# Kernel optimization log

Measured on AMD Instinct MI355X. Metric: run time of the kernel, lower is better.

## Reference

```python
import jax, jax.numpy as jnp
import numpy as np
from math import sqrt, log

B, P, C = 8, 256, 512          # batch, patch_size, input_channel
R, M = 64, 256                 # rule_num, model_size
VARPI_1, VARPI_2, TAU_0 = 0.01, 0.001, 0.9
EPS = float(np.finfo(np.float32).tiny)


def setup_inputs() -> dict:
    key = jax.random.key(0)
    ks = jax.random.split(key, 6)

    def xavier(k, shape):
        fan_out, fan_in = shape
        bound = sqrt(6.0 / (fan_in + fan_out))
        return jax.random.uniform(k, shape, jnp.float32, -bound, bound)

    sigma0 = sqrt(-M / (2.0 * (R + 1) * (R + 1) * log(0.5)))
    return {
        "input_data": jax.random.normal(ks[0], (B, P, C), jnp.float32),
        "Wq": xavier(ks[1], (M, P)),      "bq": jnp.zeros((M,), jnp.float32),
        "Wk": xavier(ks[2], (M * R, P)),  "bk": jnp.zeros((M * R,), jnp.float32),
        "Wv": xavier(ks[3], (M * R, P)),  "bv": jnp.zeros((M * R,), jnp.float32),
        "Wo": xavier(ks[4], (P, M)),      "bo": jnp.zeros((P,), jnp.float32),
        "sigma": jnp.full((R, M), sigma0, jnp.float32),
    }


def reference(input_data, Wq, bq, Wk, bk, Wv, bv, Wo, bo, sigma):
    tau = TAU_0 * (1.0 / (R + EPS)) ** (1.0 / M)
    x = jnp.transpose(input_data, (0, 2, 1))            # [B,C,P]
    q = x @ Wq.T + bq                                   # [B,C,M]
    k = (x @ Wk.T + bk).reshape(B, C, R, M)
    v = (x @ Wv.T + bv).reshape(B, C, R, M)

    dist = (q[:, :, None, :] - k) / (sigma + EPS)       # [B,C,R,M]
    fire = jnp.exp(-0.5 / M * jnp.sum(dist * dist, axis=-1)) + EPS   # [B,C,R]
    nfs = fire / (jnp.sum(fire, axis=-1, keepdims=True) + EPS)

    # nucleus-style top-p mask over rule dim (no grad)
    s = jax.lax.stop_gradient(nfs)
    sorted_desc = -jnp.sort(-s, axis=-1)
    err = jnp.cumsum(sorted_desc, axis=-1) - tau
    err = jnp.where(err < 0, jnp.ones_like(err), err)
    idx = jnp.argmin(err, axis=-1)                      # [B,C]
    thresh = jnp.take_along_axis(sorted_desc, idx[..., None], axis=-1)  # [B,C,1]
    mask = (s >= thresh).astype(jnp.float32)

    nfs = nfs * mask
    nfs = nfs / (jnp.sum(nfs, axis=-1, keepdims=True) + EPS)

    pred = jnp.einsum('bcr,bcrm->bcm', nfs, v)          # dropout is identity in eval
    out = jnp.transpose(pred @ Wo.T + bo, (0, 2, 1))    # [B,P,C]

    # constraint loss
    eye = jnp.eye(M, dtype=jnp.float32)
    weight_loss = jnp.linalg.norm(Wq @ Wo - eye)
    bias_loss = jnp.linalg.norm(bq) + jnp.linalg.norm(bo)
    key_l1 = jnp.sum(jnp.abs(Wk)) + jnp.sum(jnp.abs(bk))
    val_l1 = jnp.sum(jnp.abs(Wv)) + jnp.sum(jnp.abs(bv))
    loss = VARPI_1 * (weight_loss + bias_loss) + VARPI_2 * (key_l1 + val_l1)
    return out, loss
```

## Files before the change

### kernel.cpp

```cpp
#include <hip/hip_runtime.h>
#include <math.h>

#define EPS_F 1.1754943508222875e-38f

typedef __attribute__((ext_vector_type(8))) _Float16 half8;
typedef __attribute__((ext_vector_type(4))) float f32x4;
typedef __attribute__((ext_vector_type(8))) unsigned short ushort8;

__device__ __forceinline__ unsigned short f2h(float f) {
  _Float16 h = (_Float16)f;
  return __builtin_bit_cast(unsigned short, h);
}
__device__ __forceinline__ float h2f(unsigned short u) {
  return (float)__builtin_bit_cast(_Float16, u);
}

__device__ __forceinline__ void gload16(const void* g, void* l) {
  __builtin_amdgcn_global_load_lds(
      (const __attribute__((address_space(1))) void*)g,
      (__attribute__((address_space(3))) void*)l, 16, 0, 0);
}

__global__ __launch_bounds__(256) void k_prep_x(const float* __restrict__ in,
                                                unsigned short* __restrict__ x) {
  __shared__ float t[32][33];
  int c0 = blockIdx.x * 32, p0 = blockIdx.y * 32, b = blockIdx.z;
  int tx = threadIdx.x & 31, ty = threadIdx.x >> 5;
#pragma unroll
  for (int i = ty; i < 32; i += 8)
    t[i][tx] = in[(b * 256 + p0 + i) * 512 + c0 + tx];
  __syncthreads();
#pragma unroll
  for (int i = ty; i < 32; i += 8)
    x[(b * 512 + c0 + i) * 256 + p0 + tx] = f2h(t[tx][i]);
}

__global__ __launch_bounds__(256) void k_prepwt(
    const float* __restrict__ Wq, const float* __restrict__ Wk,
    const float* __restrict__ Wv, const float* __restrict__ Wo,
    const float* __restrict__ bq, const float* __restrict__ bk,
    const float* __restrict__ sigma,
    unsigned short* __restrict__ wd, unsigned short* __restrict__ woh,
    unsigned short* __restrict__ wqh, float* __restrict__ bdr,
    float* __restrict__ pbk, unsigned short* __restrict__ wvT,
    unsigned short* __restrict__ woT, float* __restrict__ pbv) {
  __shared__ float t[32][33];
  __shared__ float r1[4];
  const int bid = blockIdx.x;
  const int lane = threadIdx.x & 63, w = threadIdx.x >> 6;
  if (bid < 4096) {
    int gid = bid * 256 + threadIdx.x;
    int i4 = gid * 4;
    int rm = i4 >> 8, p = i4 & 255, m = rm & 255;
    const float4 wk = *(const float4*)(Wk + i4);
    const float4 wq = *(const float4*)(Wq + m * 256 + p);
    float rs = 1.0f / (sigma[rm] + EPS_F);
    ushort4 d;
    d.x = f2h((wq.x - wk.x) * rs); d.y = f2h((wq.y - wk.y) * rs);
    d.z = f2h((wq.z - wk.z) * rs); d.w = f2h((wq.w - wk.w) * rs);
    *(ushort4*)(wd + i4) = d;
    float ak = fabsf(wk.x) + fabsf(wk.y) + fabsf(wk.z) + fabsf(wk.w);
    if (p == 0) bdr[rm] = (bq[m] - bk[rm]) * rs;
    if (gid < 65536) {
      woh[gid] = f2h(Wo[gid]);
      ushort4 q4;
      q4.x = f2h(wq.x); q4.y = f2h(wq.y); q4.z = f2h(wq.z); q4.w = f2h(wq.w);
      *(ushort4*)(wqh + i4) = q4;
    }
#pragma unroll
    for (int dlt = 1; dlt < 64; dlt <<= 1) ak += __shfl_xor(ak, dlt);
    if (lane == 0) r1[w] = ak;
    __syncthreads();
    if (threadIdx.x == 0)
      pbk[bid] = r1[0] + r1[1] + r1[2] + r1[3];
  } else {
    int tt = bid - 4096;
    int z = tt >> 6, rem = tt & 63;
    int bx = rem & 7, by = rem >> 3;
    int tx = threadIdx.x & 31, ty = threadIdx.x >> 5;
    if (z < 64) {
      int p0 = bx * 32, m0 = by * 32, r = z;
      float av = 0.f;
#pragma unroll
      for (int i = ty; i < 32; i += 8) {
        float v = Wv[(size_t)(r * 256 + m0 + i) * 256 + p0 + tx];
        t[i][tx] = v;
        av += fabsf(v);
      }
      __syncthreads();
#pragma unroll
      for (int i = ty; i < 32; i += 8)
        wvT[(size_t)r * 65536 + (p0 + i) * 256 + m0 + tx] = f2h(t[tx][i]);
#pragma unroll
      for (int d = 1; d < 64; d <<= 1) av += __shfl_xor(av, d);
      if (lane == 0) r1[w] = av;
      __syncthreads();
      if (threadIdx.x == 0)
        pbv[r * 64 + by * 8 + bx] = r1[0] + r1[1] + r1[2] + r1[3];
    } else {
      int p0 = bx * 32, m0 = by * 32;
#pragma unroll
      for (int i = ty; i < 32; i += 8)
        t[i][tx] = Wo[(p0 + i) * 256 + m0 + tx];
      __syncthreads();
#pragma unroll
      for (int i = ty; i < 32; i += 8)
        woT[(m0 + i) * 256 + p0 + tx] = f2h(t[tx][i]);
    }
  }
}

__global__ __launch_bounds__(256) void k_gwx(
    const unsigned short* __restrict__ woh, const unsigned short* __restrict__ wvT,
    const unsigned short* __restrict__ wqh, const unsigned short* __restrict__ woT,
    const float* __restrict__ bv,
    unsigned short* __restrict__ G, float* __restrict__ pbw,
    float* __restrict__ hv) {
  __shared__ unsigned short As[128 * 64];
  __shared__ unsigned short Bs[128 * 64];
  __shared__ float red4[4];
  __shared__ float bvl[256];
  const int bid = blockIdx.x;
  const int tid = threadIdx.x, w = tid >> 6, lane = tid & 63;
  const int wr = w >> 1, wc = w & 1, cl = lane & 15, kg = lane >> 4;

  if (bid < 260) {
    const bool isgw = bid < 256;
    const int r = bid >> 2;
    const int rowbase = isgw ? (((bid >> 1) & 1) * 128) : (((bid - 256) >> 1) * 128);
    const int colbase = isgw ? ((bid & 1) * 128) : (((bid - 256) & 1) * 128);
    const unsigned short* Aglob = isgw ? woh : wqh;
    const unsigned short* Bglob = isgw ? (wvT + (size_t)r * 65536) : woT;

    f32x4 acc[4][4];
#pragma unroll
    for (int i = 0; i < 4; ++i)
#pragma unroll
      for (int j = 0; j < 4; ++j) acc[i][j] = (f32x4){0.f, 0.f, 0.f, 0.f};

    for (int tks = 0; tks < 4; ++tks) {
      const int kc = tks * 64;
      __syncthreads();
#pragma unroll
      for (int j = 0; j < 4; ++j) {
        int s = w * 4 + j;
        int ch = s * 64 + lane;
        int row = ch >> 3, c = ch & 7;
        gload16(Aglob + (rowbase + row) * 256 + kc + ((c ^ (row & 7)) << 3),
                As + s * 512);
        gload16(Bglob + (colbase + row) * 256 + kc + ((c ^ (row & 7)) << 3),
                Bs + s * 512);
      }
      __syncthreads();
#pragma unroll
      for (int kk = 0; kk < 2; ++kk) {
        half8 a[4], b[4];
        int g = kk * 4 + kg;
#pragma unroll
        for (int i = 0; i < 4; ++i) {
          int row = wr * 64 + i * 16 + cl;
          a[i] = *(const half8*)(As + row * 64 + ((g ^ (row & 7)) << 3));
        }
#pragma unroll
        for (int j = 0; j < 4; ++j) {
          int n = wc * 64 + j * 16 + cl;
          b[j] = *(const half8*)(Bs + n * 64 + ((g ^ (n & 7)) << 3));
        }
#pragma unroll
        for (int i = 0; i < 4; ++i)
#pragma unroll
          for (int j = 0; j < 4; ++j)
            acc[i][j] = __builtin_amdgcn_mfma_f32_16x16x32_f16(a[i], b[j], acc[i][j], 0, 0, 0);
      }
    }
    if (isgw) {
#pragma unroll
      for (int i = 0; i < 4; ++i)
#pragma unroll
        for (int q = 0; q < 4; ++q) {
          int pr = rowbase + wr * 64 + i * 16 + kg * 4 + q;
#pragma unroll
          for (int j = 0; j < 4; ++j) {
            int pc = colbase + wc * 64 + j * 16 + cl;
            G[(size_t)r * 65536 + pr * 256 + pc] = f2h(acc[i][j][q]);
          }
        }
    } else {
      float s = 0.f;
#pragma unroll
      for (int i = 0; i < 4; ++i)
#pragma unroll
        for (int q = 0; q < 4; ++q) {
          int rg = rowbase + wr * 64 + i * 16 + kg * 4 + q;
#pragma unroll
          for (int j = 0; j < 4; ++j) {
            int cg = colbase + wc * 64 + j * 16 + cl;
            float dd = acc[i][j][q] - (rg == cg ? 1.0f : 0.0f);
            s += dd * dd;
          }
        }
#pragma unroll
      for (int d = 1; d < 64; d <<= 1) s += __shfl_xor(s, d);
      if (lane == 0) red4[w] = s;
      __syncthreads();
      if (tid == 0)
        pbw[bid - 256] = red4[0] + red4[1] + red4[2] + red4[3];
    }
  } else {
    int r = bid - 260;
    bvl[tid] = bv[r * 256 + tid];
    __syncthreads();
    float s = 0.f;
#pragma unroll 8
    for (int c8 = 0; c8 < 32; ++c8) {
      ushort8 wv8 = *(const ushort8*)(woh + tid * 256 + c8 * 8);
#pragma unroll
      for (int e = 0; e < 8; ++e) s = fmaf(h2f(wv8[e]), bvl[c8 * 8 + e], s);
    }
    hv[r * 256 + tid] = s;
  }
}

__global__ __launch_bounds__(256, 2) void k_fire(
    const unsigned short* __restrict__ xh, const unsigned short* __restrict__ wd,
    const float* __restrict__ bdr, float* __restrict__ fire_p) {
  __shared__ unsigned short As[128 * 64];
  __shared__ unsigned short Bs[256 * 64];
  __shared__ float red[128][2];
  const int tid = threadIdx.x, w = tid >> 6, lane = tid & 63;
  const int wr = w >> 1, wc = w & 1, cl = lane & 15, kg = lane >> 4;
  const int wg = blockIdx.x;
  const int swz = (wg & 7) * 256 + (wg >> 3);
  const int bc0 = (swz & 31) * 128, r = swz >> 5;

  float bdrv[8];
#pragma unroll
  for (int j = 0; j < 8; ++j)
    bdrv[j] = bdr[r * 256 + wc * 128 + j * 16 + cl];

  f32x4 acc[4][8];
#pragma unroll
  for (int i = 0; i < 4; ++i)
#pragma unroll
    for (int j = 0; j < 8; ++j) acc[i][j] = (f32x4){0.f, 0.f, 0.f, 0.f};

  for (int t = 0; t < 4; ++t) {
    const int kc = t * 64;
    __syncthreads();
#pragma unroll
    for (int j = 0; j < 4; ++j) {
      int s = w * 4 + j;
      int ch = s * 64 + lane;
      int row = ch >> 3, c = ch & 7;
      gload16(xh + (size_t)(bc0 + row) * 256 + kc + ((c ^ (row & 7)) << 3),
              As + s * 512);
    }
#pragma unroll
    for (int j = 0; j < 8; ++j) {
      int s = w * 8 + j;
      int ch = s * 64 + lane;
      int n = ch >> 3, c = ch & 7;
      gload16(wd + (size_t)r * 65536 + n * 256 + kc + ((c ^ (n & 7)) << 3),
              Bs + s * 512);
    }
    __syncthreads();
#pragma unroll
    for (int kk = 0; kk < 2; ++kk) {
      half8 a[4], b[8];
      int g = kk * 4 + kg;
#pragma unroll
      for (int i = 0; i < 4; ++i) {
        int row = wr * 64 + i * 16 + cl;
        a[i] = *(const half8*)(As + row * 64 + ((g ^ (row & 7)) << 3));
      }
#pragma unroll
      for (int j = 0; j < 8; ++j) {
        int n = wc * 128 + j * 16 + cl;
        b[j] = *(const half8*)(Bs + n * 64 + ((g ^ (n & 7)) << 3));
      }
#pragma unroll
      for (int i = 0; i < 4; ++i)
#pragma unroll
        for (int j = 0; j < 8; ++j)
          acc[i][j] = __builtin_amdgcn_mfma_f32_16x16x32_f16(a[i], b[j], acc[i][j], 0, 0, 0);
    }
  }
  float rowsum[4][4];
#pragma unroll
  for (int i = 0; i < 4; ++i)
#pragma unroll
    for (int q = 0; q < 4; ++q) {
      float s2 = 0.f;
#pragma unroll
      for (int j = 0; j < 8; ++j) {
        float t2 = acc[i][j][q] + bdrv[j];
        s2 += t2 * t2;
      }
      rowsum[i][q] = s2;
    }
#pragma unroll
  for (int dlt = 1; dlt < 16; dlt <<= 1)
#pragma unroll
    for (int i = 0; i < 4; ++i)
#pragma unroll
      for (int q = 0; q < 4; ++q) rowsum[i][q] += __shfl_xor(rowsum[i][q], dlt);
  if (cl == 0) {
#pragma unroll
    for (int i = 0; i < 4; ++i)
#pragma unroll
      for (int q = 0; q < 4; ++q)
        red[wr * 64 + i * 16 + kg * 4 + q][wc] = rowsum[i][q];
  }
  __syncthreads();
  if (tid < 128)
    fire_p[(size_t)(bc0 + tid) * 64 + r] = red[tid][0] + red[tid][1];
}

__global__ __launch_bounds__(256) void k_mask(const float* __restrict__ fire_p,
                                              float* __restrict__ nfs, float tau) {
  int w = threadIdx.x >> 6, lane = threadIdx.x & 63;
  int bc = blockIdx.x * 4 + w;
  size_t ix = (size_t)bc * 64 + lane;
  float f = expf(-0.001953125f * fire_p[ix]) + EPS_F;
  float tot = f;
#pragma unroll
  for (int d = 1; d < 64; d <<= 1) tot += __shfl_xor(tot, d);
  float nf = f / (tot + EPS_F);
  float v = nf;
#pragma unroll
  for (int k = 2; k <= 64; k <<= 1) {
#pragma unroll
    for (int j = 32; j > 0; j >>= 1) {
      if (j >= k) continue;
      float o = __shfl_xor(v, j);
      bool lower = (lane & j) == 0;
      bool desc = (lane & k) == 0;
      float mn = fminf(v, o), mx = fmaxf(v, o);
      v = (desc == lower) ? mx : mn;
    }
  }
  float cs = v;
#pragma unroll
  for (int d = 1; d < 64; d <<= 1) {
    float t = __shfl_up(cs, d);
    if (lane >= d) cs += t;
  }
  float err = cs - tau;
  if (err < 0.f) err = 1.0f;
  float mn = err;
#pragma unroll
  for (int d = 1; d < 64; d <<= 1) mn = fminf(mn, __shfl_xor(mn, d));
  unsigned long long ball = __ballot(err == mn);
  int idx = __ffsll(ball) - 1;
  float thresh = __shfl(v, idx);
  float keep = (nf >= thresh) ? nf : 0.0f;
  float tot2 = keep;
#pragma unroll
  for (int d = 1; d < 64; d <<= 1) tot2 += __shfl_xor(tot2, d);
  nfs[ix] = keep / (tot2 + EPS_F);
}

__global__ __launch_bounds__(512, 4) void k_predg(
    const unsigned short* __restrict__ xh, const unsigned short* __restrict__ G,
    const float* __restrict__ nfs, const float* __restrict__ hv,
    unsigned short* __restrict__ pp) {
  __shared__ unsigned short As[128 * 64];
  __shared__ unsigned short Bs[128 * 64];
  __shared__ float nl[128][9];
  const int tid = threadIdx.x, w = tid >> 6, lane = tid & 63;
  const int wr = w >> 1, wc = w & 1, cl = lane & 15, kg = lane >> 4;
  const int wg = blockIdx.x;
  const int swz = (wg & 7) * 64 + (wg >> 3);
  const int sl = swz >> 6, inner = swz & 63;
  const int bc0 = ((inner >> 1) & 31) * 128, ph = inner & 1;

  for (int e = tid; e < 1024; e += 512)
    nl[e >> 3][e & 7] = nfs[(size_t)(bc0 + (e >> 3)) * 64 + sl * 8 + (e & 7)];

  f32x4 acc[2][4];
#pragma unroll
  for (int i = 0; i < 2; ++i)
#pragma unroll
    for (int j = 0; j < 4; ++j) acc[i][j] = (f32x4){0.f, 0.f, 0.f, 0.f};

  _Float16 nlh[2];
  for (int t = 0; t < 32; ++t) {
    const int rr = t >> 2, kc = (t & 3) * 64;
    __syncthreads();
#pragma unroll
    for (int j = 0; j < 2; ++j) {
      int s = w * 2 + j;
      int ch = s * 64 + lane;
      int row = ch >> 3, c = ch & 7;
      gload16(xh + (size_t)(bc0 + row) * 256 + kc + ((c ^ (row & 7)) << 3),
              As + s * 512);
      gload16(G + (size_t)(sl * 8 + rr) * 65536 + (ph * 128 + row) * 256 + kc +
                  ((c ^ (row & 7)) << 3),
              Bs + s * 512);
    }
    __syncthreads();
    if ((t & 3) == 0) {
#pragma unroll
      for (int i = 0; i < 2; ++i)
        nlh[i] = (_Float16)nl[wr * 32 + i * 16 + cl][rr];
    }
#pragma unroll
    for (int kk = 0; kk < 2; ++kk) {
      half8 a[2], b[4];
      int g = kk * 4 + kg;
#pragma unroll
      for (int i = 0; i < 2; ++i) {
        int row = wr * 32 + i * 16 + cl;
        a[i] = *(const half8*)(As + row * 64 + ((g ^ (row & 7)) << 3));
        a[i] = a[i] * nlh[i];
      }
#pragma unroll
      for (int j = 0; j < 4; ++j) {
        int n = wc * 64 + j * 16 + cl;
        b[j] = *(const half8*)(Bs + n * 64 + ((g ^ (n & 7)) << 3));
      }
#pragma unroll
      for (int i = 0; i < 2; ++i)
#pragma unroll
        for (int j = 0; j < 4; ++j)
          acc[i][j] = __builtin_amdgcn_mfma_f32_16x16x32_f16(a[i], b[j], acc[i][j], 0, 0, 0);
    }
  }
  float hvv[8][4];
#pragma unroll
  for (int j = 0; j < 4; ++j) {
    int col = ph * 128 + wc * 64 + j * 16 + cl;
#pragma unroll
    for (int rr = 0; rr < 8; ++rr)
      hvv[rr][j] = hv[(sl * 8 + rr) * 256 + col];
  }
  unsigned short* base = pp + (size_t)sl * 1048576;
#pragma unroll
  for (int i = 0; i < 2; ++i)
#pragma unroll
    for (int q = 0; q < 4; ++q) {
      int outrow = wr * 32 + i * 16 + kg * 4 + q;
      float nlv[8];
#pragma unroll
      for (int rr = 0; rr < 8; ++rr) nlv[rr] = nl[outrow][rr];
#pragma unroll
      for (int j = 0; j < 4; ++j) {
        float s = acc[i][j][q];
#pragma unroll
        for (int rr = 0; rr < 8; ++rr) s = fmaf(nlv[rr], hvv[rr][j], s);
        int col = ph * 128 + wc * 64 + j * 16 + cl;
        base[(size_t)(bc0 + outrow) * 256 + col] = f2h(s);
      }
    }
}

__global__ __launch_bounds__(256) void k_finalout(const unsigned short* __restrict__ pp,
                                                  const float* __restrict__ bo,
                                                  float* __restrict__ out) {
  __shared__ float sacc[256][33];
  __shared__ float bol[256];
  const int tid = threadIdx.x;
  bol[tid] = bo[tid];
  const int bc0 = blockIdx.x * 32;
  const int b = bc0 >> 9, c0 = bc0 & 511;
#pragma unroll
  for (int i = 0; i < 4; ++i) {
    int unit = tid + 256 * i;
    int pch = unit & 31, lbc = unit >> 5;
    float s[8];
#pragma unroll
    for (int e = 0; e < 8; ++e) s[e] = 0.f;
#pragma unroll
    for (int sl = 0; sl < 8; ++sl) {
      ushort8 v = *(const ushort8*)(pp + (size_t)sl * 1048576 +
                                    (size_t)(bc0 + lbc) * 256 + pch * 8);
#pragma unroll
      for (int e = 0; e < 8; ++e) s[e] += h2f(v[e]);
    }
#pragma unroll
    for (int e = 0; e < 8; ++e) sacc[pch * 8 + e][lbc] = s[e];
  }
  __syncthreads();
  const int p = tid;
  float bov = bol[p];
  float* dst = out + (size_t)b * 131072 + (size_t)p * 512 + c0;
#pragma unroll
  for (int e0 = 0; e0 < 8; ++e0) {
    float4 v;
    v.x = sacc[p][e0 * 4 + 0] + bov;
    v.y = sacc[p][e0 * 4 + 1] + bov;
    v.z = sacc[p][e0 * 4 + 2] + bov;
    v.w = sacc[p][e0 * 4 + 3] + bov;
    *(float4*)(dst + e0 * 4) = v;
  }
}

__global__ __launch_bounds__(1024) void k_final(
    const float* __restrict__ bq, const float* __restrict__ bk,
    const float* __restrict__ bv, const float* __restrict__ bo,
    const float* __restrict__ pbw, const float* __restrict__ pbk,
    const float* __restrict__ pbv, float* __restrict__ loss_out) {
  __shared__ float r[16][5];
  const int tid = threadIdx.x;
  float swq = (tid < 4) ? pbw[tid] : 0.f;
  float sbk = 0.f, sbv = 0.f;
  for (int i = tid; i < 4096; i += 1024) {
    sbk += pbk[i];
    sbv += pbv[i];
  }
  for (int i = tid; i < 16384; i += 1024) {
    sbk += fabsf(bk[i]);
    sbv += fabsf(bv[i]);
  }
  float sbq = 0.f, sbo = 0.f;
  if (tid < 256) {
    float a = bq[tid];
    sbq = a * a;
    float b = bo[tid];
    sbo = b * b;
  }
  int lane = tid & 63, w = tid >> 6;
#pragma unroll
  for (int d = 1; d < 64; d <<= 1) {
    swq += __shfl_xor(swq, d);
    sbk += __shfl_xor(sbk, d);
    sbv += __shfl_xor(sbv, d);
    sbq += __shfl_xor(sbq, d);
    sbo += __shfl_xor(sbo, d);
  }
  if (lane == 0) {
    r[w][0] = swq; r[w][1] = sbk; r[w][2] = sbv; r[w][3] = sbq; r[w][4] = sbo;
  }
  __syncthreads();
  if (tid == 0) {
    float t[5] = {0.f, 0.f, 0.f, 0.f, 0.f};
    for (int i = 0; i < 16; ++i)
      for (int j = 0; j < 5; ++j) t[j] += r[i][j];
    float loss = 0.01f * (sqrtf(t[0]) + sqrtf(t[3]) + sqrtf(t[4])) +
                 0.001f * (t[1] + t[2]);
    *loss_out = loss;
  }
}

extern "C" void kernel_launch(void* const* d_in, const int* in_sizes, int n_in,
                              void* d_out, int out_size, void* d_ws, size_t ws_size,
                              hipStream_t stream) {
  const float* in    = (const float*)d_in[0];
  const float* Wq    = (const float*)d_in[1];
  const float* bq    = (const float*)d_in[2];
  const float* Wk    = (const float*)d_in[3];
  const float* bk    = (const float*)d_in[4];
  const float* Wv    = (const float*)d_in[5];
  const float* bv    = (const float*)d_in[6];
  const float* Wo    = (const float*)d_in[7];
  const float* bo    = (const float*)d_in[8];
  const float* sigma = (const float*)d_in[9];
  float* out = (float*)d_out;

  char* ws = (char*)d_ws;
  unsigned short* xh     = (unsigned short*)(ws);
  unsigned short* woh    = (unsigned short*)(ws + 2097152);
  float*          bdr    = (float*)(ws + 2228224);
  float*          nfs    = (float*)(ws + 2293760);
  float*          fire_p = (float*)(ws + 3342336);
  float*          pbk    = (float*)(ws + 4390912);
  float*          pbv    = (float*)(ws + 4407296);
  float*          pbw    = (float*)(ws + 4423680);
  float*          hv     = (float*)(ws + 4424704);
  unsigned short* wd     = (unsigned short*)(ws + 4718592);
  unsigned short* wvT    = (unsigned short*)(ws + 13107200);
  unsigned short* pp     = (unsigned short*)(ws + 4718592);
  unsigned short* G      = (unsigned short*)(ws + 21495808);
  unsigned short* wqh    = (unsigned short*)(ws + 29884416);
  unsigned short* woT    = (unsigned short*)(ws + 30015488);

  k_prep_x<<<dim3(16, 8, 8), 256, 0, stream>>>(in, xh);
  k_prepwt<<<8256, 256, 0, stream>>>(Wq, Wk, Wv, Wo, bq, bk, sigma,
                                     wd, woh, wqh, bdr, pbk, wvT, woT, pbv);
  k_gwx<<<324, 256, 0, stream>>>(woh, wvT, wqh, woT, bv, G, pbw, hv);
  k_fire<<<2048, 256, 0, stream>>>(xh, wd, bdr, fire_p);
  const float tau = (float)(0.9 * pow(1.0 / (64.0 + (double)EPS_F), 1.0 / 256.0));
  k_mask<<<1024, 256, 0, stream>>>(fire_p, nfs, tau);
  k_predg<<<512, 512, 0, stream>>>(xh, G, nfs, hv, pp);
  k_finalout<<<128, 256, 0, stream>>>(pp, bo, out);
  k_final<<<1, 1024, 0, stream>>>(bq, bk, bv, bo, pbw, pbk, pbv, out + 1048576);
}
```

Baseline: 129.5 us.

## Double-buffer LDS tiles in k_fire and k_predg to overlap loads with MFMA

Both GEMM-style kernels now split the LDS staging buffers into two halves with a K-tile of 32 instead of 64. Each iteration prefetches the next tile into the other buffer while it computes on the current one, so only one barrier is needed per iteration. The XOR swizzle is adapted to the narrower 32-element rows. This aims to hide global-to-LDS latency behind MFMA work. The cost is twice as many iterations and barriers, with less MFMA work per barrier.

```diff
diff --git a/kernel.cpp b/kernel.cpp
--- a/kernel.cpp
+++ b/kernel.cpp
@@ -224,8 +224,8 @@
 __global__ __launch_bounds__(256, 2) void k_fire(
     const unsigned short* __restrict__ xh, const unsigned short* __restrict__ wd,
     const float* __restrict__ bdr, float* __restrict__ fire_p) {
-  __shared__ unsigned short As[128 * 64];
-  __shared__ unsigned short Bs[256 * 64];
+  __shared__ unsigned short As[2][128 * 32];
+  __shared__ unsigned short Bs[2][256 * 32];
   __shared__ float red[128][2];
   const int tid = threadIdx.x, w = tid >> 6, lane = tid & 63;
   const int wr = w >> 1, wc = w & 1, cl = lane & 15, kg = lane >> 4;
@@ -233,57 +233,61 @@
   const int swz = (wg & 7) * 256 + (wg >> 3);
   const int bc0 = (swz & 31) * 128, r = swz >> 5;
 
-  float bdrv[8];
-#pragma unroll
-  for (int j = 0; j < 8; ++j)
-    bdrv[j] = bdr[r * 256 + wc * 128 + j * 16 + cl];
-
-  f32x4 acc[4][8];
-#pragma unroll
-  for (int i = 0; i < 4; ++i)
-#pragma unroll
-    for (int j = 0; j < 8; ++j) acc[i][j] = (f32x4){0.f, 0.f, 0.f, 0.f};
-
-  for (int t = 0; t < 4; ++t) {
-    const int kc = t * 64;
-    __syncthreads();
+  auto stage = [&](int t) {
+    const int kc = t * 32;
+    unsigned short* da = (unsigned short*)As[t & 1];
+    unsigned short* db = (unsigned short*)Bs[t & 1];
+#pragma unroll
+    for (int j = 0; j < 2; ++j) {
+      int s = w * 2 + j;
+      int ch = s * 64 + lane;
+      int row = ch >> 2, c = ch & 3;
+      gload16(xh + (size_t)(bc0 + row) * 256 + kc + ((c ^ ((row >> 1) & 3)) << 3),
+              da + s * 512);
+    }
 #pragma unroll
     for (int j = 0; j < 4; ++j) {
       int s = w * 4 + j;
       int ch = s * 64 + lane;
-      int row = ch >> 3, c = ch & 7;
-      gload16(xh + (size_t)(bc0 + row) * 256 + kc + ((c ^ (row & 7)) << 3),
-              As + s * 512);
+      int n = ch >> 2, c = ch & 3;
+      gload16(wd + (size_t)r * 65536 + n * 256 + kc + ((c ^ ((n >> 1) & 3)) << 3),
+              db + s * 512);
+    }
+  };
+
+  float bdrv[8];
+#pragma unroll
+  for (int j = 0; j < 8; ++j)
+    bdrv[j] = bdr[r * 256 + wc * 128 + j * 16 + cl];
+
+  f32x4 acc[4][8];
+#pragma unroll
+  for (int i = 0; i < 4; ++i)
+#pragma unroll
+    for (int j = 0; j < 8; ++j) acc[i][j] = (f32x4){0.f, 0.f, 0.f, 0.f};
+
+  stage(0);
+  for (int t = 0; t < 8; ++t) {
+    __syncthreads();
+    if (t + 1 < 8) stage(t + 1);
+    const unsigned short* Ac = As[t & 1];
+    const unsigned short* Bc = Bs[t & 1];
+    half8 a[4], b[8];
+#pragma unroll
+    for (int i = 0; i < 4; ++i) {
+      int row = wr * 64 + i * 16 + cl;
+      a[i] = *(const half8*)(Ac + row * 32 + ((kg ^ ((row >> 1) & 3)) << 3));
     }
 #pragma unroll
     for (int j = 0; j < 8; ++j) {
-      int s = w * 8 + j;
-      int ch = s * 64 + lane;
-      int n = ch >> 3, c = ch & 7;
-      gload16(wd + (size_t)r * 65536 + n * 256 + kc + ((c ^ (n & 7)) << 3),
-              Bs + s * 512);
-    }
-    __syncthreads();
-#pragma unroll
-    for (int kk = 0; kk < 2; ++kk) {
-      half8 a[4], b[8];
-      int g = kk * 4 + kg;
-#pragma unroll
-      for (int i = 0; i < 4; ++i) {
-        int row = wr * 64 + i * 16 + cl;
-        a[i] = *(const half8*)(As + row * 64 + ((g ^ (row & 7)) << 3));
-      }
-#pragma unroll
-      for (int j = 0; j < 8; ++j) {
-        int n = wc * 128 + j * 16 + cl;
-        b[j] = *(const half8*)(Bs + n * 64 + ((g ^ (n & 7)) << 3));
-      }
-#pragma unroll
-      for (int i = 0; i < 4; ++i)
-#pragma unroll
-        for (int j = 0; j < 8; ++j)
-          acc[i][j] = __builtin_amdgcn_mfma_f32_16x16x32_f16(a[i], b[j], acc[i][j], 0, 0, 0);
-    }
+      int n = wc * 128 + j * 16 + cl;
+      b[j] = *(const half8*)(Bc + n * 32 + ((kg ^ ((n >> 1) & 3)) << 3));
+    }
+#pragma unroll
+    for (int i = 0; i < 4; ++i)
+#pragma unroll
+      for (int j = 0; j < 8; ++j)
+        acc[i][j] = __builtin_amdgcn_mfma_f32_16x16x32_f16(a[i], b[j], acc[i][j], 0, 0, 0);
   }
   float rowsum[4][4];
 #pragma unroll
@@ -364,8 +368,8 @@
     const unsigned short* __restrict__ xh, const unsigned short* __restrict__ G,
     const float* __restrict__ nfs, const float* __restrict__ hv,
     unsigned short* __restrict__ pp) {
-  __shared__ unsigned short As[128 * 64];
-  __shared__ unsigned short Bs[128 * 64];
+  __shared__ unsigned short As[2][128 * 32];
+  __shared__ unsigned short Bs[2][128 * 32];
   __shared__ float nl[128][9];
   const int tid = threadIdx.x, w = tid >> 6, lane = tid & 63;
   const int wr = w >> 1, wc = w & 1, cl = lane & 15, kg = lane >> 4;
@@ -374,6 +378,27 @@
   const int sl = swz >> 6, inner = swz & 63;
   const int bc0 = ((inner >> 1) & 31) * 128, ph = inner & 1;
 
+  auto stage = [&](int t) {
+    const int rr = t >> 3, kc = (t & 7) * 32;
+    unsigned short* da = (unsigned short*)As[t & 1];
+    unsigned short* db = (unsigned short*)Bs[t & 1];
+    {
+      int s = w;
+      int ch = s * 64 + lane;
+      int row = ch >> 2, c = ch & 3;
+      gload16(xh + (size_t)(bc0 + row) * 256 + kc + ((c ^ ((row >> 1) & 3)) << 3),
+              da + s * 512);
+    }
+    {
+      int s = w;
+      int ch = s * 64 + lane;
+      int n = ch >> 2, c = ch & 3;
+      gload16(G + (size_t)(sl * 8 + rr) * 65536 + (ph * 128 + n) * 256 + kc +
+                  ((c ^ ((n >> 1) & 3)) << 3),
+              db + s * 512);
+    }
+  };
+
   for (int e = tid; e < 1024; e += 512)
     nl[e >> 3][e & 7] = nfs[(size_t)(bc0 + (e >> 3)) * 64 + sl * 8 + (e & 7)];
 
@@ -383,48 +408,36 @@
 #pragma unroll
     for (int j = 0; j < 4; ++j) acc[i][j] = (f32x4){0.f, 0.f, 0.f, 0.f};
 
+  stage(0);
   _Float16 nlh[2];
-  for (int t = 0; t < 32; ++t) {
-    const int rr = t >> 2, kc = (t & 3) * 64;
+  for (int t = 0; t < 64; ++t) {
+    const int rr = t >> 3;
     __syncthreads();
-#pragma unroll
-    for (int j = 0; j < 2; ++j) {
-      int s = w * 2 + j;
-      int ch = s * 64 + lane;
-      int row = ch >> 3, c = ch & 7;
-      gload16(xh + (size_t)(bc0 + row) * 256 + kc + ((c ^ (row & 7)) << 3),
-              As + s * 512);
-      gload16(G + (size_t)(sl * 8 + rr) * 65536 + (ph * 128 + row) * 256 + kc +
-                  ((c ^ (row & 7)) << 3),
-              Bs + s * 512);
-    }
-    __syncthreads();
-    if ((t & 3) == 0) {
+    if (t + 1 < 64) stage(t + 1);
+    if ((t & 7) == 0) {
 #pragma unroll
       for (int i = 0; i < 2; ++i)
         nlh[i] = (_Float16)nl[wr * 32 + i * 16 + cl][rr];
     }
-#pragma unroll
-    for (int kk = 0; kk < 2; ++kk) {
-      half8 a[2], b[4];
-      int g = kk * 4 + kg;
-#pragma unroll
-      for (int i = 0; i < 2; ++i) {
-        int row = wr * 32 + i * 16 + cl;
-        a[i] = *(const half8*)(As + row * 64 + ((g ^ (row & 7)) << 3));
-        a[i] = a[i] * nlh[i];
-      }
-#pragma unroll
-      for (int j = 0; j < 4; ++j) {
-        int n = wc * 64 + j * 16 + cl;
-        b[j] = *(const half8*)(Bs + n * 64 + ((g ^ (n & 7)) << 3));
-      }
-#pragma unroll
-      for (int i = 0; i < 2; ++i)
-#pragma unroll
-        for (int j = 0; j < 4; ++j)
-          acc[i][j] = __builtin_amdgcn_mfma_f32_16x16x32_f16(a[i], b[j], acc[i][j], 0, 0, 0);
-    }
+    const unsigned short* Ac = As[t & 1];
+    const unsigned short* Bc = Bs[t & 1];
+    half8 a[2], b[4];
+#pragma unroll
+    for (int i = 0; i < 2; ++i) {
+      int row = wr * 32 + i * 16 + cl;
+      a[i] = *(const half8*)(Ac + row * 32 + ((kg ^ ((row >> 1) & 3)) << 3));
+      a[i] = a[i] * nlh[i];
+    }
+#pragma unroll
+    for (int j = 0; j < 4; ++j) {
+      int n = wc * 64 + j * 16 + cl;
+      b[j] = *(const half8*)(Bc + n * 32 + ((kg ^ ((n >> 1) & 3)) << 3));
+    }
+#pragma unroll
+    for (int i = 0; i < 2; ++i)
+#pragma unroll
+      for (int j = 0; j < 4; ++j)
+        acc[i][j] = __builtin_amdgcn_mfma_f32_16x16x32_f16(a[i], b[j], acc[i][j], 0, 0, 0);
   }
   float hvv[8][4];
 #pragma unroll
```

Measured after the change: 136.8 us. 5.6% more time.
